# Optimization experiments

Hardware: AMD Instinct MI355X
Metric: run time of the kernel (lower is better)

The kernel has to match this reference:

```python
import jax, jax.numpy as jnp
import numpy as np

B, T, D_MODEL, H, D = 2, 2048, 2048, 16, 128


def _rope_tables(t, d_half, base=10000.0):
    inv_freq = 1.0 / (base ** (jnp.arange(d_half, dtype=jnp.float32) / d_half))
    ang = jnp.arange(t, dtype=jnp.float32)[:, None] * inv_freq[None, :]  # (T, D/2)
    return jnp.cos(ang), jnp.sin(ang)


def setup_inputs() -> dict:
    key = jax.random.key(0)
    ks = jax.random.split(key, 5)
    x = jax.random.normal(ks[0], (B, T, D_MODEL), dtype=jnp.float32)
    mask = jnp.tril(jnp.ones((T, T), dtype=bool))  # causal boolean mask
    cos, sin = _rope_tables(T, D // 2)
    std = 1.0 / np.sqrt(D_MODEL)
    Wq = jax.random.normal(ks[1], (D_MODEL, H * D), dtype=jnp.float32) * std
    Wk = jax.random.normal(ks[2], (D_MODEL, H * D), dtype=jnp.float32) * std
    Wv = jax.random.normal(ks[3], (D_MODEL, H * D), dtype=jnp.float32) * std
    Wo = jax.random.normal(ks[4], (H * D, D_MODEL), dtype=jnp.float32) * std
    return {"x": x, "mask": mask, "cos": cos, "sin": sin,
            "Wq": Wq, "Wk": Wk, "Wv": Wv, "Wo": Wo}


def _apply_rope(x, cos, sin):
    # x: (B, H, T, D); cos/sin: (T, D/2)
    half = x.shape[-1] // 2
    x1, x2 = x[..., :half], x[..., half:]
    c = cos[None, None]
    s = sin[None, None]
    return jnp.concatenate([x1 * c - x2 * s, x1 * s + x2 * c], axis=-1)


def reference(x, mask, cos, sin, Wq, Wk, Wv, Wo):
    b, t, _ = x.shape
    scale = 1.0 / np.sqrt(D)
    # projections: (B, T, H*D) -> (B, H, T, D)
    q = (x @ Wq).reshape(b, t, H, D).transpose(0, 2, 1, 3)
    k = (x @ Wk).reshape(b, t, H, D).transpose(0, 2, 1, 3)
    v = (x @ Wv).reshape(b, t, H, D).transpose(0, 2, 1, 3)
    q = _apply_rope(q, cos, sin)
    k = _apply_rope(k, cos, sin)
    scores = jnp.einsum('bhqd,bhkd->bhqk', q, k) * scale
    scores = jnp.where(mask[None, None], scores, jnp.float32(-1e30))
    attn = jax.nn.softmax(scores, axis=-1)
    out = jnp.einsum('bhqk,bhkd->bhqd', attn, v)  # (B, H, T, D)
    out = out.transpose(0, 2, 1, 3).reshape(b, t, H * D)
    return out @ Wo
```

## Files before the change

### kernel.cpp

```cpp
#include <hip/hip_runtime.h>

#define T_SEQ 2048
#define DM    2048
#define NH    16
#define HD    128
#define NROW  4096

typedef __attribute__((ext_vector_type(8))) short short8;
typedef __attribute__((ext_vector_type(4))) float f32x4;
typedef __attribute__((ext_vector_type(16))) float f32x16;

static __device__ __forceinline__ float bf2f(unsigned short h) {
    unsigned int u = ((unsigned int)h) << 16;
    return __builtin_bit_cast(float, u);
}
static __device__ __forceinline__ unsigned short f2bf(float f) {
    unsigned int u = __builtin_bit_cast(unsigned int, f);
    u += 0x7FFFu + ((u >> 16) & 1u);
    return (unsigned short)(u >> 16);
}
static __device__ __forceinline__ unsigned short bf_fast(float f) {
    return (unsigned short)((__builtin_bit_cast(unsigned int, f) + 0x8000u) >> 16);
}
static __device__ __forceinline__ unsigned int pk2(float lo, float hi) {
    return (unsigned int)bf_fast(lo) | ((unsigned int)bf_fast(hi) << 16);
}

typedef __attribute__((address_space(1))) const unsigned int gas_uint;
typedef __attribute__((address_space(3))) unsigned int las_uint;

static __device__ __forceinline__ void load_lds16(const void* g, void* l) {
    __builtin_amdgcn_global_load_lds((gas_uint*)g, (las_uint*)l, 16, 0, 0);
}

static __device__ __forceinline__ f32x4 mfma_bf16(short8 a, short8 b, f32x4 c) {
    return __builtin_amdgcn_mfma_f32_16x16x32_bf16(a, b, c, 0, 0, 0);
}
static __device__ __forceinline__ f32x16 mfma32_bf16(short8 a, short8 b, f32x16 c) {
    return __builtin_amdgcn_mfma_f32_32x32x16_bf16(a, b, c, 0, 0, 0);
}

__global__ __launch_bounds__(256) void k_prep(const float* __restrict__ x,
                                              unsigned short* __restrict__ xb,
                                              const float* __restrict__ w0, const float* __restrict__ w1,
                                              const float* __restrict__ w2, const float* __restrict__ w3,
                                              unsigned short* __restrict__ t0, unsigned short* __restrict__ t1,
                                              unsigned short* __restrict__ t2, unsigned short* __restrict__ t3) {
    const int tid = threadIdx.x;
    const int z = blockIdx.z;
    if (z == 4) {
        const int iblock = blockIdx.y * 32 + blockIdx.x;
#pragma unroll
        for (int i = 0; i < 8; ++i) {
            int idx = (iblock * 2048 + i * 256 + tid) * 4;
            float4 v = *(const float4*)(x + idx);
            ushort4 o;
            o.x = f2bf(v.x); o.y = f2bf(v.y); o.z = f2bf(v.z); o.w = f2bf(v.w);
            *(ushort4*)(xb + idx) = o;
        }
        return;
    }
    __shared__ unsigned short tile[64][68];
    const float* W = (z == 0) ? w0 : (z == 1) ? w1 : (z == 2) ? w2 : w3;
    unsigned short* Wt = (z == 0) ? t0 : (z == 1) ? t1 : (z == 2) ? t2 : t3;
    const int bx = blockIdx.x * 64;
    const int by = blockIdx.y * 64;
    const int rr = tid >> 4, cc = (tid & 15) * 4;
#pragma unroll
    for (int it = 0; it < 4; ++it) {
        int row = it * 16 + rr;
        float4 v = *(const float4*)(W + (size_t)(by + row) * DM + bx + cc);
        ushort4 o;
        o.x = f2bf(v.x); o.y = f2bf(v.y); o.z = f2bf(v.z); o.w = f2bf(v.w);
        *(ushort4*)&tile[row][cc] = o;
    }
    __syncthreads();
#pragma unroll
    for (int it = 0; it < 4; ++it) {
        int ln = it * 16 + rr;
        ushort4 v;
#pragma unroll
        for (int j = 0; j < 4; ++j) v = (j == 0) ? (ushort4){tile[cc][ln], 0, 0, 0} : v, ((unsigned short*)&v)[j] = tile[cc + j][ln];
        *(ushort4*)(Wt + (size_t)(bx + ln) * DM + by + cc) = v;
    }
}

template <int MODE>
static __device__ __forceinline__ void gemm_body(unsigned short* smem,
                                                 const unsigned short* __restrict__ A,
                                                 const unsigned short* __restrict__ Bt,
                                                 unsigned short* __restrict__ Cb,
                                                 float* __restrict__ Cf,
                                                 const float* __restrict__ cosp,
                                                 const float* __restrict__ sinp,
                                                 int m0i, int n0i) {
    unsigned short* As = smem;
    unsigned short* Bs = smem + 8192;
    const int tid = threadIdx.x;
    const int w = tid >> 6, lane = tid & 63;
    const int col = lane & 15, quad = lane >> 4;
    const int wm = w >> 1, wn = w & 1;
    const size_t m0 = (size_t)m0i;
    const size_t n0 = (size_t)n0i;

    f32x4 acc[4][4];
#pragma unroll
    for (int i = 0; i < 4; ++i)
#pragma unroll
        for (int j = 0; j < 4; ++j)
            acc[i][j] = (f32x4){0.f, 0.f, 0.f, 0.f};

    const int lrow = lane >> 3;
    const int gcol = ((lane & 7) ^ lrow) * 8;

    for (int k0 = 0; k0 < DM; k0 += 64) {
#pragma unroll
        for (int c = w; c < 16; c += 4) {
            load_lds16(A + (m0 + c * 8 + lrow) * DM + k0 + gcol, &As[c * 512]);
            load_lds16(Bt + (n0 + c * 8 + lrow) * DM + k0 + gcol, &Bs[c * 512]);
        }
        __syncthreads();
#pragma unroll
        for (int ks = 0; ks < 2; ++ks) {
            short8 af[4], bf[4];
            int g = ks * 4 + quad;
#pragma unroll
            for (int mt = 0; mt < 4; ++mt) {
                int r = wm * 64 + mt * 16 + col;
                af[mt] = *(const short8*)&As[r * 64 + ((g ^ (r & 7)) * 8)];
            }
#pragma unroll
            for (int nt = 0; nt < 4; ++nt) {
                int r = wn * 64 + nt * 16 + col;
                bf[nt] = *(const short8*)&Bs[r * 64 + ((g ^ (r & 7)) * 8)];
            }
#pragma unroll
            for (int mt = 0; mt < 4; ++mt)
#pragma unroll
                for (int nt = 0; nt < 4; ++nt)
                    acc[mt][nt] = mfma_bf16(af[mt], bf[nt], acc[mt][nt]);
        }
        __syncthreads();
    }

    if (MODE == 0 || MODE == 1) {
#pragma unroll
        for (int mt = 0; mt < 4; ++mt)
#pragma unroll
            for (int nt = 0; nt < 4; ++nt)
#pragma unroll
                for (int reg = 0; reg < 4; ++reg) {
                    size_t r = m0 + wm * 64 + mt * 16 + quad * 4 + reg;
                    size_t c = n0 + wn * 64 + nt * 16 + col;
                    if (MODE == 1) Cf[r * DM + c] = acc[mt][nt][reg];
                    else           Cb[r * DM + c] = f2bf(acc[mt][nt][reg]);
                }
    } else if (MODE == 2) {
        unsigned short* tile = smem;
        const int tbl = wm * 64 + quad * 4;
#pragma unroll
        for (int mt = 0; mt < 4; ++mt)
#pragma unroll
            for (int nt = 0; nt < 4; ++nt) {
                const int cl = wn * 64 + nt * 16 + col;
                ushort4 v;
#pragma unroll
                for (int reg = 0; reg < 4; ++reg)
                    ((unsigned short*)&v)[reg] = f2bf(acc[mt][nt][reg]);
                *(ushort4*)&tile[cl * 132 + tbl + mt * 16] = v;
            }
        __syncthreads();
        const int bb = m0i >> 11;
        const int tg = m0i & 2047;
#pragma unroll
        for (int i = 0; i < 16; ++i) {
            const int task = i * 256 + tid;
            const int cl = task >> 5;
            const int tp = (task & 31) * 4;
            ushort4 v = *(const ushort4*)&tile[cl * 132 + tp];
            *(ushort4*)(Cb + (size_t)(bb * 2048 + n0i + cl) * T_SEQ + tg + tp) = v;
        }
    } else {
        unsigned short* tile = smem;
#pragma unroll
        for (int mt = 0; mt < 4; ++mt)
#pragma unroll
            for (int nt = 0; nt < 4; ++nt)
#pragma unroll
                for (int reg = 0; reg < 4; ++reg) {
                    const int rl = wm * 64 + mt * 16 + quad * 4 + reg;
                    const int cl = wn * 64 + nt * 16 + col;
                    tile[rl * 132 + cl] = f2bf(acc[mt][nt][reg]);
                }
        __syncthreads();
#pragma unroll
        for (int i = 0; i < 8; ++i) {
            const int task = i * 256 + tid;
            const int rl = task >> 4;
            const int d4 = (task & 15) * 4;
            const int r = m0i + rl;
            const int t = r & (T_SEQ - 1);
            ushort4 x1 = *(const ushort4*)&tile[rl * 132 + d4];
            ushort4 x2 = *(const ushort4*)&tile[rl * 132 + d4 + 64];
            float4 c = *(const float4*)(cosp + t * 64 + d4);
            float4 s = *(const float4*)(sinp + t * 64 + d4);
            ushort4 o1, o2;
#pragma unroll
            for (int q = 0; q < 4; ++q) {
                float a1 = bf2f(((const unsigned short*)&x1)[q]);
                float a2 = bf2f(((const unsigned short*)&x2)[q]);
                float cc = ((const float*)&c)[q], ss = ((const float*)&s)[q];
                ((unsigned short*)&o1)[q] = f2bf(a1 * cc - a2 * ss);
                ((unsigned short*)&o2)[q] = f2bf(a1 * ss + a2 * cc);
            }
            *(ushort4*)(Cb + (size_t)r * DM + n0 + d4)      = o1;
            *(ushort4*)(Cb + (size_t)r * DM + n0 + d4 + 64) = o2;
        }
    }
}

__global__ __launch_bounds__(256) void k_gemm_qkv(const unsigned short* __restrict__ xb,
                                                  const unsigned short* __restrict__ wtq,
                                                  const unsigned short* __restrict__ wtk,
                                                  const unsigned short* __restrict__ wtv,
                                                  unsigned short* __restrict__ qb,
                                                  unsigned short* __restrict__ kb,
                                                  unsigned short* __restrict__ vt,
                                                  const float* __restrict__ cosp,
                                                  const float* __restrict__ sinp) {
    __shared__ unsigned short smem[16896];
    const int f = blockIdx.x;
    const int xcd = f & 7, i = f >> 3;
    const int z = i >> 6, idx = i & 63;
    const int tx = (xcd & 1) * 8 + (idx & 7);
    const int ty = (xcd >> 1) * 8 + (idx >> 3);
    const int m0i = ty * 128, n0i = tx * 128;
    if (z == 0)      gemm_body<0>(smem, xb, wtq, qb, nullptr, nullptr, nullptr, m0i, n0i);
    else if (z == 1) gemm_body<3>(smem, xb, wtk, kb, nullptr, cosp, sinp, m0i, n0i);
    else             gemm_body<2>(smem, xb, wtv, vt, nullptr, nullptr, nullptr, m0i, n0i);
}

__global__ __launch_bounds__(256) void k_gemm_out(const unsigned short* __restrict__ ob,
                                                  const unsigned short* __restrict__ wto,
                                                  float* __restrict__ out) {
    __shared__ unsigned short smem[16384];
    const int f = blockIdx.x;
    const int xcd = f & 7, idx = f >> 3;
    const int tx = (xcd & 1) * 8 + (idx & 7);
    const int ty = (xcd >> 1) * 8 + (idx >> 3);
    gemm_body<1>(smem, ob, wto, nullptr, out, nullptr, nullptr, ty * 128, tx * 128);
}

__global__ __launch_bounds__(256) void k_flash(const unsigned short* __restrict__ Q,
                                               const unsigned short* __restrict__ K,
                                               const unsigned short* __restrict__ Vt,
                                               unsigned short* __restrict__ O,
                                               const float* __restrict__ cosp,
                                               const float* __restrict__ sinp) {
    __shared__ unsigned short Ks[64 * 128];
    __shared__ unsigned short Vs[128 * 64];
    const int tid = threadIdx.x;
    const int w = tid >> 6, lane = tid & 63;
    const int col = lane & 31, l5 = lane >> 5;
    const int flat = blockIdx.x | (blockIdx.y << 4) | (blockIdx.z << 8);
    const int j = 15 - (flat >> 5);
    const int hb = flat & 31;
    const int h = hb & 15, b = hb >> 4;
    const int q0 = j * 128;
    const size_t rowbase = ((size_t)b * T_SEQ) * DM + (size_t)h * HD;
    const size_t hbase = ((size_t)b * NH + h) * HD;
    const float SCL = 0.088388347648318447f * 1.4426950408889634f;

    const int t = q0 + w * 32 + col;
    short8 qf[8];
    {
        const unsigned short* qp = Q + rowbase + (size_t)t * DM + l5 * 8;
#pragma unroll
        for (int st = 0; st < 8; ++st)
            qf[st] = *(const short8*)(qp + st * 16);
        const float* cp = cosp + t * 64 + l5 * 8;
        const float* sp = sinp + t * 64 + l5 * 8;
#pragma unroll
        for (int st = 0; st < 4; ++st) {
            float4 c0 = *(const float4*)(cp + st * 16);
            float4 c1 = *(const float4*)(cp + st * 16 + 4);
            float4 s0v = *(const float4*)(sp + st * 16);
            float4 s1v = *(const float4*)(sp + st * 16 + 4);
#pragma unroll
            for (int jj = 0; jj < 8; ++jj) {
                float cv = ((jj < 4) ? ((const float*)&c0)[jj] : ((const float*)&c1)[jj - 4]) * SCL;
                float sv = ((jj < 4) ? ((const float*)&s0v)[jj] : ((const float*)&s1v)[jj - 4]) * SCL;
                float a1 = bf2f((unsigned short)qf[st][jj]);
                float a2 = bf2f((unsigned short)qf[st + 4][jj]);
                qf[st][jj]     = (short)f2bf(a1 * cv - a2 * sv);
                qf[st + 4][jj] = (short)f2bf(a1 * sv + a2 * cv);
            }
        }
    }

    f32x16 o[4];
#pragma unroll
    for (int i = 0; i < 4; ++i) o[i] = (f32x16)(0.f);
    float m_i = -1e30f, l_i = 0.f;

    const int kt_max = 2 * j + 1;
    const int kt_lim = (q0 + w * 32 + 31) >> 6;
    const int cswz = col & 7;

    for (int kt = 0; kt <= kt_max; ++kt) {
        const int k0 = kt * 64;
        __syncthreads();
#pragma unroll
        for (int c = 0; c < 4; ++c) {
            const int c4 = w * 4 + c;
            const int krow = c4 * 4 + (lane >> 4);
            const int kpos = lane & 15;
            load_lds16(K + rowbase + (size_t)(k0 + krow) * DM + ((kpos ^ (krow & 7)) * 8),
                       &Ks[c4 * 512]);
            const int vrow = c4 * 8 + (lane >> 3);
            const int vpos = lane & 7;
            load_lds16(Vt + (hbase + vrow) * (size_t)T_SEQ + k0 + ((vpos ^ (vrow & 7)) * 8),
                       &Vs[c4 * 512]);
        }
        __syncthreads();
        if (kt > kt_lim) continue;

        f32x16 s0 = (f32x16)(0.f), s1 = (f32x16)(0.f);
#pragma unroll
        for (int st = 0; st < 8; ++st) {
            const int dg = (2 * st + l5) ^ cswz;
            short8 kf0 = *(const short8*)&Ks[col * 128 + dg * 8];
            short8 kf1 = *(const short8*)&Ks[col * 128 + 4096 + dg * 8];
            s0 = mfma32_bf16(kf0, qf[st], s0);
            s1 = mfma32_bf16(kf1, qf[st], s1);
        }

        if (k0 + 63 > q0 + w * 32) {
            const int kb = k0 + 4 * l5;
#pragma unroll
            for (int r = 0; r < 16; ++r) {
                const int key = kb + (r & 3) + 8 * (r >> 2);
                if (key > t) s0[r] = -1e30f;
                if (key + 32 > t) s1[r] = -1e30f;
            }
        }

        float mx = -1e30f;
#pragma unroll
        for (int r = 0; r < 16; ++r) mx = fmaxf(mx, fmaxf(s0[r], s1[r]));
        mx = fmaxf(mx, __shfl_xor(mx, 32));
        if (!__all(mx - m_i <= 8.0f)) {
            const float mnew = fmaxf(m_i, mx);
            const float alpha = __builtin_amdgcn_exp2f(m_i - mnew);
            m_i = mnew;
            l_i *= alpha;
#pragma unroll
            for (int i = 0; i < 4; ++i) o[i] *= alpha;
        }
        float sum = 0.f;
#pragma unroll
        for (int r = 0; r < 16; ++r) {
            float p0 = __builtin_amdgcn_exp2f(s0[r] - m_i);
            float p1 = __builtin_amdgcn_exp2f(s1[r] - m_i);
            s0[r] = p0; s1[r] = p1;
            sum += p0 + p1;
        }
        sum += __shfl_xor(sum, 32);
        l_i += sum;

        short8 pb[4];
#pragma unroll
        for (int st = 0; st < 2; ++st) {
            {
                unsigned pA0 = pk2(s0[8 * st + 0], s0[8 * st + 1]);
                unsigned pA1 = pk2(s0[8 * st + 2], s0[8 * st + 3]);
                unsigned pB0 = pk2(s0[8 * st + 4], s0[8 * st + 5]);
                unsigned pB1 = pk2(s0[8 * st + 6], s0[8 * st + 7]);
                unsigned sa = l5 ? pA0 : pB0, sb = l5 ? pA1 : pB1;
                unsigned ra = __shfl_xor(sa, 32), rb = __shfl_xor(sb, 32);
                unsigned oa = l5 ? pB0 : pA0, ob = l5 ? pB1 : pA1;
                uint4 wv = {l5 ? ra : oa, l5 ? rb : ob, l5 ? oa : ra, l5 ? ob : rb};
                pb[st] = __builtin_bit_cast(short8, wv);
            }
            {
                unsigned pA0 = pk2(s1[8 * st + 0], s1[8 * st + 1]);
                unsigned pA1 = pk2(s1[8 * st + 2], s1[8 * st + 3]);
                unsigned pB0 = pk2(s1[8 * st + 4], s1[8 * st + 5]);
                unsigned pB1 = pk2(s1[8 * st + 6], s1[8 * st + 7]);
                unsigned sa = l5 ? pA0 : pB0, sb = l5 ? pA1 : pB1;
                unsigned ra = __shfl_xor(sa, 32), rb = __shfl_xor(sb, 32);
                unsigned oa = l5 ? pB0 : pA0, ob = l5 ? pB1 : pA1;
                uint4 wv = {l5 ? ra : oa, l5 ? rb : ob, l5 ? oa : ra, l5 ? ob : rb};
                pb[st + 2] = __builtin_bit_cast(short8, wv);
            }
        }

#pragma unroll
        for (int ms = 0; ms < 4; ++ms) {
            const int drow = (ms * 32 + col) * 64;
#pragma unroll
            for (int st = 0; st < 4; ++st) {
                const int kg = (2 * st + l5) ^ cswz;
                short8 vf = *(const short8*)&Vs[drow + kg * 8];
                o[ms] = mfma32_bf16(vf, pb[st], o[ms]);
            }
        }
    }

    const float inv = __builtin_amdgcn_rcpf(l_i);
    unsigned short* op = O + rowbase + (size_t)t * DM;
#pragma unroll
    for (int ms = 0; ms < 4; ++ms)
#pragma unroll
        for (int g = 0; g < 4; ++g) {
            ushort4 st4;
#pragma unroll
            for (int i = 0; i < 4; ++i)
                ((unsigned short*)&st4)[i] = bf_fast(o[ms][g * 4 + i] * inv);
            *(ushort4*)(op + ms * 32 + g * 8 + 4 * l5) = st4;
        }
}

extern "C" void kernel_launch(void* const* d_in, const int* in_sizes, int n_in,
                              void* d_out, int out_size, void* d_ws, size_t ws_size,
                              hipStream_t stream) {
    const float* x    = (const float*)d_in[0];
    const float* cosp = (const float*)d_in[2];
    const float* sinp = (const float*)d_in[3];
    const float* Wq   = (const float*)d_in[4];
    const float* Wk   = (const float*)d_in[5];
    const float* Wv   = (const float*)d_in[6];
    const float* Wo   = (const float*)d_in[7];
    float* out = (float*)d_out;

    unsigned short* xb  = (unsigned short*)d_ws;
    unsigned short* wtq = xb  + (size_t)NROW * DM;
    unsigned short* wtk = wtq + (size_t)DM * DM;
    unsigned short* wtv = wtk + (size_t)DM * DM;
    unsigned short* wto = wtv + (size_t)DM * DM;
    unsigned short* qb  = wto + (size_t)DM * DM;
    unsigned short* kb  = qb  + (size_t)NROW * DM;
    unsigned short* vt  = kb  + (size_t)NROW * DM;
    unsigned short* ob  = vt  + (size_t)NROW * DM;

    hipLaunchKernelGGL(k_prep, dim3(32, 32, 5), dim3(256), 0, stream,
                       x, xb, Wq, Wk, Wv, Wo, wtq, wtk, wtv, wto);
    hipLaunchKernelGGL(k_gemm_qkv, dim3(1536), dim3(256), 0, stream,
                       xb, wtq, wtk, wtv, qb, kb, vt, cosp, sinp);
    hipLaunchKernelGGL(k_flash, dim3(16, 16, 2), dim3(256), 0, stream,
                       qb, kb, vt, ob, cosp, sinp);
    hipLaunchKernelGGL(k_gemm_out, dim3(512), dim3(256), 0, stream, ob, wto, out);
}
```

Measured before the change: 369.9 us.

## Double-buffer K/V tiles in flash attention to overlap loads with compute

Splits the K and V shared-memory tiles into two buffers and prefetches the next key block while computing on the current one. This replaces the two barriers per iteration with a single barrier at the end. The aim is to hide global-to-LDS load latency behind the QK and PV MFMA work. It doubles LDS use per block, which may reduce occupancy.

Result: slower. 379.4 us (+2.6%).

```diff
diff --git a/kernel.cpp b/kernel.cpp
--- a/kernel.cpp
+++ b/kernel.cpp
@@ -257,8 +257,8 @@
                                                unsigned short* __restrict__ O,
                                                const float* __restrict__ cosp,
                                                const float* __restrict__ sinp) {
-    __shared__ unsigned short Ks[64 * 128];
-    __shared__ unsigned short Vs[128 * 64];
+    __shared__ unsigned short Ks[2][64 * 128];
+    __shared__ unsigned short Vs[2][128 * 64];
     const int tid = threadIdx.x;
     const int w = tid >> 6, lane = tid & 63;
     const int col = lane & 31, l5 = lane >> 5;
@@ -272,6 +272,24 @@
     const float SCL = 0.088388347648318447f * 1.4426950408889634f;
 
     const int t = q0 + w * 32 + col;
+    const int krow_l = (lane >> 4);
+    const int kpos = lane & 15;
+    const int vrow_l = (lane >> 3);
+    const int vpos = lane & 7;
+
+#define STAGE_KV(bf_, k0_) do {                                                          \
+    _Pragma("unroll")                                                                    \
+    for (int c = 0; c < 4; ++c) {                                                        \
+        const int c4 = w * 4 + c;                                                        \
+        const int krow = c4 * 4 + krow_l;                                                \
+        load_lds16(K + rowbase + (size_t)((k0_) + krow) * DM + ((kpos ^ (krow & 7)) * 8),\
+                   &Ks[bf_][c4 * 512]);                                                  \
+        const int vrow = c4 * 8 + vrow_l;                                                \
+        load_lds16(Vt + (hbase + vrow) * (size_t)T_SEQ + (k0_) + ((vpos ^ (vrow & 7)) * 8),\
+                   &Vs[bf_][c4 * 512]);                                                  \
+    }                                                                                    \
+} while (0)
+
     short8 qf[8];
     {
         const unsigned short* qp = Q + rowbase + (size_t)t * DM + l5 * 8;
@@ -307,105 +325,100 @@
     const int kt_lim = (q0 + w * 32 + 31) >> 6;
     const int cswz = col & 7;
 
+    STAGE_KV(0, 0);
+    __syncthreads();
+
     for (int kt = 0; kt <= kt_max; ++kt) {
-        const int k0 = kt * 64;
+        const int buf = kt & 1;
+        if (kt < kt_max) STAGE_KV(buf ^ 1, (kt + 1) * 64);
+
+        if (kt <= kt_lim) {
+            const int k0 = kt * 64;
+            f32x16 s0 = (f32x16)(0.f), s1 = (f32x16)(0.f);
+#pragma unroll
+            for (int st = 0; st < 8; ++st) {
+                const int dg = (2 * st + l5) ^ cswz;
+                short8 kf0 = *(const short8*)&Ks[buf][col * 128 + dg * 8];
+                short8 kf1 = *(const short8*)&Ks[buf][col * 128 + 4096 + dg * 8];
+                s0 = mfma32_bf16(kf0, qf[st], s0);
+                s1 = mfma32_bf16(kf1, qf[st], s1);
+            }
+
+            if (k0 + 63 > q0 + w * 32) {
+                const int kb = k0 + 4 * l5;
+#pragma unroll
+                for (int r = 0; r < 16; ++r) {
+                    const int key = kb + (r & 3) + 8 * (r >> 2);
+                    if (key > t) s0[r] = -1e30f;
+                    if (key + 32 > t) s1[r] = -1e30f;
+                }
+            }
+
+            float mx = -1e30f;
+#pragma unroll
+            for (int r = 0; r < 16; ++r) mx = fmaxf(mx, fmaxf(s0[r], s1[r]));
+            mx = fmaxf(mx, __shfl_xor(mx, 32));
+            if (!__all(mx - m_i <= 8.0f)) {
+                const float mnew = fmaxf(m_i, mx);
+                const float alpha = __builtin_amdgcn_exp2f(m_i - mnew);
+                m_i = mnew;
+                l_i *= alpha;
+#pragma unroll
+                for (int i = 0; i < 4; ++i) o[i] *= alpha;
+            }
+            float sum = 0.f;
+#pragma unroll
+            for (int r = 0; r < 16; ++r) {
+                float p0 = __builtin_amdgcn_exp2f(s0[r] - m_i);
+                float p1 = __builtin_amdgcn_exp2f(s1[r] - m_i);
+                s0[r] = p0; s1[r] = p1;
+                sum += p0 + p1;
+            }
+            sum += __shfl_xor(sum, 32);
+            l_i += sum;
+
+            short8 pb[4];
+#pragma unroll
+            for (int st = 0; st < 2; ++st) {
+                {
+                    unsigned pA0 = pk2(s0[8 * st + 0], s0[8 * st + 1]);
+                    unsigned pA1 = pk2(s0[8 * st + 2], s0[8 * st + 3]);
+                    unsigned pB0 = pk2(s0[8 * st + 4], s0[8 * st + 5]);
+                    unsigned pB1 = pk2(s0[8 * st + 6], s0[8 * st + 7]);
+                    unsigned sa = l5 ? pA0 : pB0, sb = l5 ? pA1 : pB1;
+                    unsigned ra = __shfl_xor(sa, 32), rb = __shfl_xor(sb, 32);
+                    unsigned oa = l5 ? pB0 : pA0, ob = l5 ? pB1 : pA1;
+                    uint4 wv = {l5 ? ra : oa, l5 ? rb : ob, l5 ? oa : ra, l5 ? ob : rb};
+                    pb[st] = __builtin_bit_cast(short8, wv);
+                }
+                {
+                    unsigned pA0 = pk2(s1[8 * st + 0], s1[8 * st + 1]);
+                    unsigned pA1 = pk2(s1[8 * st + 2], s1[8 * st + 3]);
+                    unsigned pB0 = pk2(s1[8 * st + 4], s1[8 * st + 5]);
+                    unsigned pB1 = pk2(s1[8 * st + 6], s1[8 * st + 7]);
+                    unsigned sa = l5 ? pA0 : pB0, sb = l5 ? pA1 : pB1;
+                    unsigned ra = __shfl_xor(sa, 32), rb = __shfl_xor(sb, 32);
+                    unsigned oa = l5 ? pB0 : pA0, ob = l5 ? pB1 : pA1;
+                    uint4 wv = {l5 ? ra : oa, l5 ? rb : ob, l5 ? oa : ra, l5 ? ob : rb};
+                    pb[st + 2] = __builtin_bit_cast(short8, wv);
+                }
+            }
+
+#pragma unroll
+            for (int ms = 0; ms < 4; ++ms) {
+                const int drow = (ms * 32 + col) * 64;
+#pragma unroll
+                for (int st = 0; st < 4; ++st) {
+                    const int kg = (2 * st + l5) ^ cswz;
+                    short8 vf = *(const short8*)&Vs[buf][drow + kg * 8];
+                    o[ms] = mfma32_bf16(vf, pb[st], o[ms]);
+                }
+            }
+        }
+
         __syncthreads();
-#pragma unroll
-        for (int c = 0; c < 4; ++c) {
-            const int c4 = w * 4 + c;
-            const int krow = c4 * 4 + (lane >> 4);
-            const int kpos = lane & 15;
-            load_lds16(K + rowbase + (size_t)(k0 + krow) * DM + ((kpos ^ (krow & 7)) * 8),
-                       &Ks[c4 * 512]);
-            const int vrow = c4 * 8 + (lane >> 3);
-            const int vpos = lane & 7;
-            load_lds16(Vt + (hbase + vrow) * (size_t)T_SEQ + k0 + ((vpos ^ (vrow & 7)) * 8),
-                       &Vs[c4 * 512]);
-        }
-        __syncthreads();
-        if (kt > kt_lim) continue;
-
-        f32x16 s0 = (f32x16)(0.f), s1 = (f32x16)(0.f);
-#pragma unroll
-        for (int st = 0; st < 8; ++st) {
-            const int dg = (2 * st + l5) ^ cswz;
-            short8 kf0 = *(const short8*)&Ks[col * 128 + dg * 8];
-            short8 kf1 = *(const short8*)&Ks[col * 128 + 4096 + dg * 8];
-            s0 = mfma32_bf16(kf0, qf[st], s0);
-            s1 = mfma32_bf16(kf1, qf[st], s1);
-        }
-
-        if (k0 + 63 > q0 + w * 32) {
-            const int kb = k0 + 4 * l5;
-#pragma unroll
-            for (int r = 0; r < 16; ++r) {
-                const int key = kb + (r & 3) + 8 * (r >> 2);
-                if (key > t) s0[r] = -1e30f;
-                if (key + 32 > t) s1[r] = -1e30f;
-            }
-        }
-
-        float mx = -1e30f;
-#pragma unroll
-        for (int r = 0; r < 16; ++r) mx = fmaxf(mx, fmaxf(s0[r], s1[r]));
-        mx = fmaxf(mx, __shfl_xor(mx, 32));
-        if (!__all(mx - m_i <= 8.0f)) {
-            const float mnew = fmaxf(m_i, mx);
-            const float alpha = __builtin_amdgcn_exp2f(m_i - mnew);
-            m_i = mnew;
-            l_i *= alpha;
-#pragma unroll
-            for (int i = 0; i < 4; ++i) o[i] *= alpha;
-        }
-        float sum = 0.f;
-#pragma unroll
-        for (int r = 0; r < 16; ++r) {
-            float p0 = __builtin_amdgcn_exp2f(s0[r] - m_i);
-            float p1 = __builtin_amdgcn_exp2f(s1[r] - m_i);
-            s0[r] = p0; s1[r] = p1;
-            sum += p0 + p1;
-        }
-        sum += __shfl_xor(sum, 32);
-        l_i += sum;
-
-        short8 pb[4];
-#pragma unroll
-        for (int st = 0; st < 2; ++st) {
-            {
-                unsigned pA0 = pk2(s0[8 * st + 0], s0[8 * st + 1]);
-                unsigned pA1 = pk2(s0[8 * st + 2], s0[8 * st + 3]);
-                unsigned pB0 = pk2(s0[8 * st + 4], s0[8 * st + 5]);
-                unsigned pB1 = pk2(s0[8 * st + 6], s0[8 * st + 7]);
-                unsigned sa = l5 ? pA0 : pB0, sb = l5 ? pA1 : pB1;
-                unsigned ra = __shfl_xor(sa, 32), rb = __shfl_xor(sb, 32);
-                unsigned oa = l5 ? pB0 : pA0, ob = l5 ? pB1 : pA1;
-                uint4 wv = {l5 ? ra : oa, l5 ? rb : ob, l5 ? oa : ra, l5 ? ob : rb};
-                pb[st] = __builtin_bit_cast(short8, wv);
-            }
-            {
-                unsigned pA0 = pk2(s1[8 * st + 0], s1[8 * st + 1]);
-                unsigned pA1 = pk2(s1[8 * st + 2], s1[8 * st + 3]);
-                unsigned pB0 = pk2(s1[8 * st + 4], s1[8 * st + 5]);
-                unsigned pB1 = pk2(s1[8 * st + 6], s1[8 * st + 7]);
-                unsigned sa = l5 ? pA0 : pB0, sb = l5 ? pA1 : pB1;
-                unsigned ra = __shfl_xor(sa, 32), rb = __shfl_xor(sb, 32);
-                unsigned oa = l5 ? pB0 : pA0, ob = l5 ? pB1 : pA1;
-                uint4 wv = {l5 ? ra : oa, l5 ? rb : ob, l5 ? oa : ra, l5 ? ob : rb};
-                pb[st + 2] = __builtin_bit_cast(short8, wv);
-            }
-        }
-
-#pragma unroll
-        for (int ms = 0; ms < 4; ++ms) {
-            const int drow = (ms * 32 + col) * 64;
-#pragma unroll
-            for (int st = 0; st < 4; ++st) {
-                const int kg = (2 * st + l5) ^ cswz;
-                short8 vf = *(const short8*)&Vs[drow + kg * 8];
-                o[ms] = mfma32_bf16(vf, pb[st], o[ms]);
-            }
-        }
-    }
+    }
+#undef STAGE_KV
 
     const float inv = __builtin_amdgcn_rcpf(l_i);
     unsigned short* op = O + rowbase + (size_t)t * DM;
```
